# Optimization experiments

Measured on AMD Instinct MI355X. Metric: run time of the kernel, lower is better.

Reference implementation:

```python
import jax, jax.numpy as jnp
import numpy as np

N = 16384      # nodes (256 chess boards x 64 squares)
E = 393216     # edges (avg degree 24)
G = 256        # graphs
HID = 128
H = 4
C = 32         # head dim
L = 8          # 4 blocks x 2 GATv2Conv
NODE_DIM = 21
EDGE_DIM = 6


def setup_inputs() -> dict:
    key = jax.random.key(0)
    ks = jax.random.split(key, 12)
    x = jax.random.normal(ks[0], (N, NODE_DIM), jnp.float32)
    edge_index = jax.random.randint(ks[1], (2, E), 0, N, dtype=jnp.int32)
    edge_attr = jax.random.uniform(ks[2], (E, EDGE_DIM), dtype=jnp.float32)
    batch = jnp.sort(jax.random.randint(ks[3], (N,), 0, G, dtype=jnp.int32))

    def w(k, shape, fan_in):
        return jax.random.normal(k, shape, jnp.float32) * (1.0 / np.sqrt(fan_in))

    Win = w(ks[4], (NODE_DIM, HID), NODE_DIM)
    b_in = jnp.zeros((HID,), jnp.float32)
    Wl = w(ks[5], (L, HID, HID), HID)
    bl = jnp.zeros((L, HID), jnp.float32)
    Wr = w(ks[6], (L, HID, HID), HID)
    br = jnp.zeros((L, HID), jnp.float32)
    We = w(ks[7], (L, EDGE_DIM, HID), EDGE_DIM)
    att = w(ks[8], (L, H, C), C)
    bconv = jnp.zeros((L, HID), jnp.float32)
    gamma = jnp.ones((L, HID), jnp.float32)
    beta = jnp.zeros((L, HID), jnp.float32)
    W1 = w(ks[9], (HID, 64), HID)
    b1 = jnp.zeros((64,), jnp.float32)
    W2 = w(ks[10], (64, 3), 64)
    b2 = jnp.zeros((3,), jnp.float32)
    return dict(x=x, edge_index=edge_index, edge_attr=edge_attr, batch=batch,
                Win=Win, b_in=b_in, Wl=Wl, bl=bl, Wr=Wr, br=br, We=We, att=att,
                bconv=bconv, gamma=gamma, beta=beta, W1=W1, b1=b1, W2=W2, b2=b2)


def _gatv2(h, src, dst, ea, Wl, bl, Wr, br, We, att, bias):
    # PyG GATv2Conv: message j->i uses x_j from lin_l, x_i from lin_r
    xl = (h @ Wl + bl).reshape(N, H, C)
    xr = (h @ Wr + br).reshape(N, H, C)
    ee = (ea @ We).reshape(-1, H, C)
    m = jax.nn.leaky_relu(xl[src] + xr[dst] + ee, 0.2)   # [Ef, H, C]
    s = jnp.einsum('ehc,hc->eh', m, att)                 # [Ef, H]
    smax = jax.ops.segment_max(s, dst, num_segments=N)   # self-loops => no empty segs
    ex = jnp.exp(s - smax[dst])
    den = jax.ops.segment_sum(ex, dst, num_segments=N)
    alpha = ex / den[dst]                                # edge softmax per target node
    out = jax.ops.segment_sum(alpha[:, :, None] * xl[src], dst, num_segments=N)
    return out.reshape(N, HID) + bias


def _bn(x, g, b):
    mu = jnp.mean(x, axis=0)
    var = jnp.var(x, axis=0)
    return g * (x - mu) * jax.lax.rsqrt(var + 1e-5) + b


def reference(x, edge_index, edge_attr, batch, Win, b_in, Wl, bl, Wr, br, We, att,
              bconv, gamma, beta, W1, b1, W2, b2):
    src0, dst0 = edge_index[0], edge_index[1]
    # add self-loops with fill_value='mean' (per-target mean of incoming edge_attr)
    deg = jax.ops.segment_sum(jnp.ones((E,), jnp.float32), dst0, num_segments=N)
    loop_attr = jax.ops.segment_sum(edge_attr, dst0, num_segments=N) / jnp.maximum(deg, 1.0)[:, None]
    idx = jnp.arange(N, dtype=src0.dtype)
    src = jnp.concatenate([src0, idx])
    dst = jnp.concatenate([dst0, idx])
    ea = jnp.concatenate([edge_attr, loop_attr], axis=0)

    h = jax.nn.relu(x @ Win + b_in)
    for blk in range(4):
        res = h
        l = 2 * blk
        h = jax.nn.relu(_bn(_gatv2(h, src, dst, ea, Wl[l], bl[l], Wr[l], br[l], We[l], att[l], bconv[l]), gamma[l], beta[l]))
        l = 2 * blk + 1
        h = _bn(_gatv2(h, src, dst, ea, Wl[l], bl[l], Wr[l], br[l], We[l], att[l], bconv[l]), gamma[l], beta[l])
        h = jax.nn.relu(h + res)

    cnt = jnp.maximum(jax.ops.segment_sum(jnp.ones((N,), jnp.float32), batch, num_segments=G), 1.0)
    pooled = jax.ops.segment_sum(h, batch, num_segments=G) / cnt[:, None]
    logits = jax.nn.relu(pooled @ W1 + b1) @ W2 + b2
    return logits
```

## Files before the change

kernel.cpp:

```cpp
#include <hip/hip_runtime.h>
#include <math.h>

constexpr int N   = 16384;
constexpr int E   = 393216;
constexpr int EF  = E + N;
constexpr int G   = 256;
constexpr int HID = 128;

__device__ __forceinline__ float red16(float x) {
    union fi { float f; int i; };
    fi a, b;
    a.f = x;
    b.i = __builtin_amdgcn_mov_dpp(a.i, 0x121, 0xf, 0xf, false); a.f += b.f;
    b.i = __builtin_amdgcn_mov_dpp(a.i, 0x122, 0xf, 0xf, false); a.f += b.f;
    b.i = __builtin_amdgcn_mov_dpp(a.i, 0x124, 0xf, 0xf, false); a.f += b.f;
    b.i = __builtin_amdgcn_mov_dpp(a.i, 0x128, 0xf, 0xf, false); a.f += b.f;
    return a.f;
}

__global__ __launch_bounds__(256) void k_hist(const int* __restrict__ dst,
                                              int* __restrict__ cnt) {
    int e = blockIdx.x * 256 + threadIdx.x;
    if (e < E) atomicAdd(&cnt[dst[e]], 1);
}

__global__ __launch_bounds__(1024) void k_scan(const int* __restrict__ cnt,
                                               int* __restrict__ row_ptr) {
    __shared__ int lds[1024];
    int t = threadIdx.x;
    int local[16];
    int s = 0;
    int base = t * 16;
#pragma unroll
    for (int q = 0; q < 16; q++) { local[q] = cnt[base + q] + 1; s += local[q]; }
    lds[t] = s;
    __syncthreads();
    for (int off = 1; off < 1024; off <<= 1) {
        int v = (t >= off) ? lds[t - off] : 0;
        __syncthreads();
        lds[t] += v;
        __syncthreads();
    }
    int run = (t == 0) ? 0 : lds[t - 1];
    if (t == 0) row_ptr[0] = 0;
#pragma unroll
    for (int q = 0; q < 16; q++) { run += local[q]; row_ptr[base + q + 1] = run; }
}

__global__ __launch_bounds__(256) void k_scatter(const int* __restrict__ src,
                                                 const int* __restrict__ dst,
                                                 const int* __restrict__ row_ptr,
                                                 int* __restrict__ fill,
                                                 int* __restrict__ csr_src,
                                                 int* __restrict__ csr_eid) {
    int e = blockIdx.x * 256 + threadIdx.x;
    if (e >= E) return;
    int d = dst[e];
    int pos = row_ptr[d] + atomicAdd(&fill[d], 1);
    csr_src[pos] = src[e];
    csr_eid[pos] = e;
}

__global__ __launch_bounds__(256) void k_selfloop(const int* __restrict__ row_ptr,
                                                  int* __restrict__ csr_src,
                                                  int* __restrict__ csr_eid) {
    int i = blockIdx.x * 256 + threadIdx.x;
    if (i >= N) return;
    int pos = row_ptr[i + 1] - 1;
    csr_src[pos] = i;
    csr_eid[pos] = E + i;
}

__global__ __launch_bounds__(256) void k_loopattr(const int* __restrict__ row_ptr,
                                                  const int* __restrict__ csr_eid,
                                                  const float* __restrict__ edge_attr,
                                                  float* __restrict__ loop_attr) {
    int i = blockIdx.x * 256 + threadIdx.x;
    if (i >= N) return;
    int e0 = row_ptr[i], e1 = row_ptr[i + 1] - 1;
    float s[6] = {0, 0, 0, 0, 0, 0};
    for (int e = e0; e < e1; e++) {
        int eid = csr_eid[e];
#pragma unroll
        for (int d = 0; d < 6; d++) s[d] += edge_attr[eid * 6 + d];
    }
    float deg = (float)(e1 - e0);
    float inv = 1.0f / fmaxf(deg, 1.0f);
#pragma unroll
    for (int d = 0; d < 6; d++) loop_attr[i * 6 + d] = s[d] * inv;
}

__global__ __launch_bounds__(256) void k_build_ea(const int* __restrict__ csr_eid,
                                                  const float* __restrict__ edge_attr,
                                                  const float* __restrict__ loop_attr,
                                                  float* __restrict__ csr_ea) {
    int p = blockIdx.x * 256 + threadIdx.x;
    if (p >= EF) return;
    int eid = csr_eid[p];
    const float* s = (eid < E) ? (edge_attr + (size_t)eid * 6)
                               : (loop_attr + (size_t)(eid - E) * 6);
    float4 a = {s[0], s[1], s[2], s[3]};
    float4 b = {s[4], s[5], 0.0f, 0.0f};
    float4* dst = (float4*)(csr_ea + (size_t)p * 8);
    dst[0] = a;
    dst[1] = b;
}

__global__ __launch_bounds__(128) void k_ingemm(const float* __restrict__ x,
                                                const float* __restrict__ Win,
                                                const float* __restrict__ b_in,
                                                float* __restrict__ h) {
    __shared__ float xs[21];
    int i = blockIdx.x;
    int c = threadIdx.x;
    if (c < 21) xs[c] = x[i * 21 + c];
    __syncthreads();
    float acc = b_in[c];
#pragma unroll
    for (int d = 0; d < 21; d++) acc += xs[d] * Win[d * HID + c];
    h[i * HID + c] = fmaxf(acc, 0.0f);
}

__global__ __launch_bounds__(256) void k_gemm_lr(const float* __restrict__ h,
                                                 const float* __restrict__ Wl,
                                                 const float* __restrict__ bl,
                                                 const float* __restrict__ Wr,
                                                 const float* __restrict__ br,
                                                 float* __restrict__ XL,
                                                 float* __restrict__ XR) {
    __shared__ float hs[16][HID];
    int t = threadIdx.x;
    int r0 = blockIdx.x * 16;
    {
        int row = t >> 4;
        int col = (t & 15) * 8;
        const float4* src = (const float4*)&h[(size_t)(r0 + row) * HID + col];
        float4* dst = (float4*)&hs[row][col];
        dst[0] = src[0];
        dst[1] = src[1];
    }
    __syncthreads();
    bool right = t >= 128;
    int cp = (t & 63) * 2;
    int rbase = ((t >> 6) & 1) * 8;
    const float* W    = right ? Wr : Wl;
    const float* bias = right ? br : bl;
    float* OUT        = right ? XR : XL;
    float b0 = bias[cp], b1 = bias[cp + 1];
    float acc0[8], acc1[8];
#pragma unroll
    for (int r = 0; r < 8; r++) { acc0[r] = b0; acc1[r] = b1; }
    for (int k = 0; k < HID; k += 4) {
        float4 h4[8];
#pragma unroll
        for (int r = 0; r < 8; r++) h4[r] = *(const float4*)&hs[rbase + r][k];
#pragma unroll
        for (int kk = 0; kk < 4; kk++) {
            float2 w = *(const float2*)&W[(size_t)(k + kk) * HID + cp];
#pragma unroll
            for (int r = 0; r < 8; r++) {
                float hv = ((const float*)&h4[r])[kk];
                acc0[r] = fmaf(hv, w.x, acc0[r]);
                acc1[r] = fmaf(hv, w.y, acc1[r]);
            }
        }
    }
#pragma unroll
    for (int r = 0; r < 8; r++) {
        float2 o = {acc0[r], acc1[r]};
        *(float2*)&OUT[(size_t)(r0 + rbase + r) * HID + cp] = o;
    }
}

__global__ __launch_bounds__(256) void k_edge(const int* __restrict__ row_ptr,
                                              const int* __restrict__ csr_src,
                                              const float* __restrict__ csr_ea,
                                              const float* __restrict__ xl,
                                              const float* __restrict__ xr,
                                              const float* __restrict__ We_l,
                                              const float* __restrict__ att_l,
                                              float* __restrict__ gout) {
    int wave = (blockIdx.x * blockDim.x + threadIdx.x) >> 6;
    int lane = threadIdx.x & 63;
    if (wave >= N) return;
    int i = wave;
    int hh = lane >> 4;
    int ss = lane & 15;
    int ch0 = hh * 32 + 2 * ss;

    float2 xr2 = *(const float2*)&xr[(size_t)i * HID + ch0];
    float a0 = att_l[ch0], a1 = att_l[ch0 + 1];
    float we0[6], we1[6];
#pragma unroll
    for (int d = 0; d < 6; d++) {
        float2 w = *(const float2*)&We_l[d * HID + ch0];
        we0[d] = w.x;
        we1[d] = w.y;
    }

    float rm = -INFINITY, rd = 0.0f, acc0 = 0.0f, acc1 = 0.0f;

    int e0 = __builtin_amdgcn_readfirstlane(row_ptr[i]);
    int e1 = __builtin_amdgcn_readfirstlane(row_ptr[i + 1]);

    for (int e = e0; e < e1; e += 4) {
        float p[4], v0[4], v1[4];
#pragma unroll
        for (int k = 0; k < 4; k++) {
            int ee = e + k;
            int ec = (ee < e1) ? ee : (e1 - 1);
            int j = __builtin_amdgcn_readfirstlane(csr_src[ec]);
            const float4* ea4 = (const float4*)(csr_ea + (size_t)ec * 8);
            float4 eaA = ea4[0];
            float4 eaB = ea4[1];
            float2 xl2 = *(const float2*)&xl[(size_t)j * HID + ch0];
            float s0 = eaA.x * we0[0], s1 = eaA.x * we1[0];
            s0 = fmaf(eaA.y, we0[1], s0); s1 = fmaf(eaA.y, we1[1], s1);
            s0 = fmaf(eaA.z, we0[2], s0); s1 = fmaf(eaA.z, we1[2], s1);
            s0 = fmaf(eaA.w, we0[3], s0); s1 = fmaf(eaA.w, we1[3], s1);
            s0 = fmaf(eaB.x, we0[4], s0); s1 = fmaf(eaB.x, we1[4], s1);
            s0 = fmaf(eaB.y, we0[5], s0); s1 = fmaf(eaB.y, we1[5], s1);
            float m0 = xl2.x + xr2.x + s0;
            float m1 = xl2.y + xr2.y + s1;
            m0 = fmaxf(m0, 0.2f * m0);
            m1 = fmaxf(m1, 0.2f * m1);
            float pv = m0 * a0;
            pv = fmaf(m1, a1, pv);
            pv = red16(pv);
            p[k] = (ee < e1) ? pv : -INFINITY;
            v0[k] = xl2.x;
            v1[k] = xl2.y;
        }
        float bm = fmaxf(fmaxf(p[0], p[1]), fmaxf(p[2], p[3]));
        float nm = fmaxf(rm, bm);
        float sc = __expf(rm - nm);
        rd *= sc; acc0 *= sc; acc1 *= sc;
#pragma unroll
        for (int k = 0; k < 4; k++) {
            float ek = __expf(p[k] - nm);
            rd += ek;
            acc0 = fmaf(ek, v0[k], acc0);
            acc1 = fmaf(ek, v1[k], acc1);
        }
        rm = nm;
    }
    float inv = 1.0f / rd;
    float2 o = {acc0 * inv, acc1 * inv};
    *(float2*)&gout[(size_t)i * HID + ch0] = o;
}

__global__ __launch_bounds__(256) void k_bnstats(const float* __restrict__ v,
                                                 float* __restrict__ sums) {
    __shared__ float l_s[256], l_q[256];
    int t = threadIdx.x;
    int c = t & 127;
    int half = t >> 7;
    int r = blockIdx.x * 128 + half;
    float s = 0.0f, q = 0.0f;
    for (int it = 0; it < 64; it++, r += 2) {
        float val = v[(size_t)r * HID + c];
        s += val;
        q += val * val;
    }
    l_s[t] = s; l_q[t] = q;
    __syncthreads();
    if (t < 128) {
        s = l_s[t] + l_s[t + 128];
        q = l_q[t] + l_q[t + 128];
        atomicAdd(&sums[c], s);
        atomicAdd(&sums[128 + c], q);
    }
}

__global__ __launch_bounds__(256) void k_bnapply(const float* __restrict__ g,
                                                 const float* __restrict__ sums,
                                                 const float* __restrict__ gamma,
                                                 const float* __restrict__ beta,
                                                 const float* __restrict__ res,
                                                 float* __restrict__ out) {
    int idx4 = (blockIdx.x * 256 + threadIdx.x) * 4;
    int c = idx4 & 127;
    const float invN = 1.0f / (float)N;
    float4 gv = *(const float4*)&g[idx4];
    float4 s4 = *(const float4*)&sums[c];
    float4 q4 = *(const float4*)&sums[128 + c];
    float4 gm = *(const float4*)&gamma[c];
    float4 bt = *(const float4*)&beta[c];
    float4 o;
    {
        float mean = s4.x * invN, var = q4.x * invN - mean * mean;
        o.x = gm.x * (gv.x - mean) * rsqrtf(var + 1e-5f) + bt.x;
        mean = s4.y * invN; var = q4.y * invN - mean * mean;
        o.y = gm.y * (gv.y - mean) * rsqrtf(var + 1e-5f) + bt.y;
        mean = s4.z * invN; var = q4.z * invN - mean * mean;
        o.z = gm.z * (gv.z - mean) * rsqrtf(var + 1e-5f) + bt.z;
        mean = s4.w * invN; var = q4.w * invN - mean * mean;
        o.w = gm.w * (gv.w - mean) * rsqrtf(var + 1e-5f) + bt.w;
    }
    if (res) {
        float4 r4 = *(const float4*)&res[idx4];
        o.x += r4.x; o.y += r4.y; o.z += r4.z; o.w += r4.w;
    }
    o.x = fmaxf(o.x, 0.0f);
    o.y = fmaxf(o.y, 0.0f);
    o.z = fmaxf(o.z, 0.0f);
    o.w = fmaxf(o.w, 0.0f);
    *(float4*)&out[idx4] = o;
}

__global__ __launch_bounds__(128) void k_pool(const float* __restrict__ h,
                                              const int* __restrict__ batch,
                                              const float* __restrict__ W1,
                                              const float* __restrict__ b1,
                                              const float* __restrict__ W2,
                                              const float* __restrict__ b2,
                                              float* __restrict__ out) {
    __shared__ float pooled[HID];
    __shared__ float hid[64];
    __shared__ int bounds[2];
    int g = blockIdx.x;
    int t = threadIdx.x;
    if (t < 2) {
        int target = g + t;
        int lo = 0, hi = N;
        while (lo < hi) {
            int mid = (lo + hi) >> 1;
            if (batch[mid] < target) lo = mid + 1; else hi = mid;
        }
        bounds[t] = lo;
    }
    __syncthreads();
    int s = bounds[0], e = bounds[1];
    float acc = 0.0f;
    for (int r = s; r < e; r++) acc += h[(size_t)r * HID + t];
    float cntf = fmaxf((float)(e - s), 1.0f);
    pooled[t] = acc / cntf;
    __syncthreads();
    if (t < 64) {
        float a = b1[t];
#pragma unroll 4
        for (int c = 0; c < HID; c++) a += pooled[c] * W1[c * 64 + t];
        hid[t] = fmaxf(a, 0.0f);
    }
    __syncthreads();
    if (t < 3) {
        float a = b2[t];
#pragma unroll
        for (int j = 0; j < 64; j++) a += hid[j] * W2[j * 3 + t];
        out[g * 3 + t] = a;
    }
}

extern "C" void kernel_launch(void* const* d_in, const int* in_sizes, int n_in,
                              void* d_out, int out_size, void* d_ws, size_t ws_size,
                              hipStream_t stream) {
    const float* x         = (const float*)d_in[0];
    const int*   edge_index= (const int*)d_in[1];
    const float* edge_attr = (const float*)d_in[2];
    const int*   batch     = (const int*)d_in[3];
    const float* Win       = (const float*)d_in[4];
    const float* b_in      = (const float*)d_in[5];
    const float* Wl        = (const float*)d_in[6];
    const float* bl        = (const float*)d_in[7];
    const float* Wr        = (const float*)d_in[8];
    const float* br        = (const float*)d_in[9];
    const float* We        = (const float*)d_in[10];
    const float* att       = (const float*)d_in[11];
    const float* gamma     = (const float*)d_in[13];
    const float* beta      = (const float*)d_in[14];
    const float* W1        = (const float*)d_in[15];
    const float* b1        = (const float*)d_in[16];
    const float* W2        = (const float*)d_in[17];
    const float* b2        = (const float*)d_in[18];
    float* out = (float*)d_out;

    const int* src0 = edge_index;
    const int* dst0 = edge_index + E;

    char* ws = (char*)d_ws;
    size_t off = 0;
    auto alloc = [&](size_t bytes) -> void* {
        void* p = ws + off;
        off += (bytes + 255) & ~(size_t)255;
        return p;
    };
    int*   cnt       = (int*)alloc((size_t)2 * N * sizeof(int));
    int*   fill      = cnt + N;
    float* bnsums    = (float*)alloc((size_t)8 * 256 * sizeof(float));
    int*   row_ptr   = (int*)alloc((size_t)(N + 1) * sizeof(int));
    int*   csr_src   = (int*)alloc((size_t)EF * sizeof(int));
    int*   csr_eid   = (int*)alloc((size_t)EF * sizeof(int));
    float* csr_ea    = (float*)alloc((size_t)EF * 8 * sizeof(float));
    float* loop_attr = (float*)alloc((size_t)N * 6 * sizeof(float));
    float* H0        = (float*)alloc((size_t)N * HID * sizeof(float));
    float* H1        = (float*)alloc((size_t)N * HID * sizeof(float));
    float* XL        = (float*)alloc((size_t)N * HID * sizeof(float));
    float* XR        = (float*)alloc((size_t)N * HID * sizeof(float));
    float* GOUT      = (float*)alloc((size_t)N * HID * sizeof(float));

    hipMemsetAsync(cnt, 0, (size_t)2 * N * sizeof(int) + 8 * 256 * sizeof(float),
                   stream);
    k_hist<<<(E + 255) / 256, 256, 0, stream>>>(dst0, cnt);
    k_scan<<<1, 1024, 0, stream>>>(cnt, row_ptr);
    k_scatter<<<(E + 255) / 256, 256, 0, stream>>>(src0, dst0, row_ptr, fill,
                                                   csr_src, csr_eid);
    k_selfloop<<<(N + 255) / 256, 256, 0, stream>>>(row_ptr, csr_src, csr_eid);
    k_loopattr<<<(N + 255) / 256, 256, 0, stream>>>(row_ptr, csr_eid, edge_attr,
                                                    loop_attr);
    k_build_ea<<<(EF + 255) / 256, 256, 0, stream>>>(csr_eid, edge_attr,
                                                     loop_attr, csr_ea);
    k_ingemm<<<N, 128, 0, stream>>>(x, Win, b_in, H0);

    for (int l = 0; l < 8; l++) {
        const float* hin = (l % 2 == 0) ? H0 : H1;
        k_gemm_lr<<<N / 16, 256, 0, stream>>>(hin,
                                              Wl + (size_t)l * HID * HID, bl + l * HID,
                                              Wr + (size_t)l * HID * HID, br + l * HID,
                                              XL, XR);
        k_edge<<<N / 4, 256, 0, stream>>>(row_ptr, csr_src, csr_ea,
                                          XL, XR,
                                          We + (size_t)l * 6 * HID,
                                          att + (size_t)l * HID, GOUT);
        float* bns = bnsums + l * 256;
        k_bnstats<<<128, 256, 0, stream>>>(GOUT, bns);
        if (l % 2 == 0) {
            k_bnapply<<<(N * HID) / 1024, 256, 0, stream>>>(GOUT, bns,
                                                            gamma + l * HID,
                                                            beta + l * HID,
                                                            nullptr, H1);
        } else {
            k_bnapply<<<(N * HID) / 1024, 256, 0, stream>>>(GOUT, bns,
                                                            gamma + l * HID,
                                                            beta + l * HID,
                                                            H0, H0);
        }
    }
    k_pool<<<G, 128, 0, stream>>>(H0, batch, W1, b1, W2, b2, out);
}
```

Measured before the change: 753.8 us.

## Fuse BN-apply into GEMM, prefetch xl gathers, fold loop-attr into histogram

The even-layer BatchNorm+ReLU is now applied inside the next layer's k_gemm_lr while it loads the tile into LDS. This drops one full-tensor bnapply pass and the H1 buffer. The edge kernel double-buffers the xl gathers four edges ahead so the loads overlap with the softmax math. The self-loop attribute sum is computed with atomics in k_hist, removing the k_loopattr kernel, and k_bnstats uses 256 blocks instead of 128. The cost is extra float atomics and recomputing the BN scale and shift in every GEMM block.

```diff
diff --git a/kernel.cpp b/kernel.cpp
--- a/kernel.cpp
+++ b/kernel.cpp
@@ -19,9 +19,16 @@
 }
 
 __global__ __launch_bounds__(256) void k_hist(const int* __restrict__ dst,
-                                              int* __restrict__ cnt) {
+                                              const float* __restrict__ edge_attr,
+                                              int* __restrict__ cnt,
+                                              float* __restrict__ loopsum) {
     int e = blockIdx.x * 256 + threadIdx.x;
-    if (e < E) atomicAdd(&cnt[dst[e]], 1);
+    if (e >= E) return;
+    int d = dst[e];
+    atomicAdd(&cnt[d], 1);
+#pragma unroll
+    for (int q = 0; q < 6; q++)
+        atomicAdd(&loopsum[d * 6 + q], edge_attr[e * 6 + q]);
 }
 
 __global__ __launch_bounds__(1024) void k_scan(const int* __restrict__ cnt,
@@ -71,36 +78,27 @@
     csr_eid[pos] = E + i;
 }
 
-__global__ __launch_bounds__(256) void k_loopattr(const int* __restrict__ row_ptr,
-                                                  const int* __restrict__ csr_eid,
+__global__ __launch_bounds__(256) void k_build_ea(const int* __restrict__ csr_eid,
+                                                  const int* __restrict__ row_ptr,
                                                   const float* __restrict__ edge_attr,
-                                                  float* __restrict__ loop_attr) {
-    int i = blockIdx.x * 256 + threadIdx.x;
-    if (i >= N) return;
-    int e0 = row_ptr[i], e1 = row_ptr[i + 1] - 1;
-    float s[6] = {0, 0, 0, 0, 0, 0};
-    for (int e = e0; e < e1; e++) {
-        int eid = csr_eid[e];
-#pragma unroll
-        for (int d = 0; d < 6; d++) s[d] += edge_attr[eid * 6 + d];
-    }
-    float deg = (float)(e1 - e0);
-    float inv = 1.0f / fmaxf(deg, 1.0f);
-#pragma unroll
-    for (int d = 0; d < 6; d++) loop_attr[i * 6 + d] = s[d] * inv;
-}
-
-__global__ __launch_bounds__(256) void k_build_ea(const int* __restrict__ csr_eid,
-                                                  const float* __restrict__ edge_attr,
-                                                  const float* __restrict__ loop_attr,
+                                                  const float* __restrict__ loopsum,
                                                   float* __restrict__ csr_ea) {
     int p = blockIdx.x * 256 + threadIdx.x;
     if (p >= EF) return;
     int eid = csr_eid[p];
-    const float* s = (eid < E) ? (edge_attr + (size_t)eid * 6)
-                               : (loop_attr + (size_t)(eid - E) * 6);
-    float4 a = {s[0], s[1], s[2], s[3]};
-    float4 b = {s[4], s[5], 0.0f, 0.0f};
+    float4 a, b;
+    if (eid < E) {
+        const float* s = edge_attr + (size_t)eid * 6;
+        a = {s[0], s[1], s[2], s[3]};
+        b = {s[4], s[5], 0.0f, 0.0f};
+    } else {
+        int i = eid - E;
+        float deg = (float)(row_ptr[i + 1] - row_ptr[i] - 1);
+        float inv = 1.0f / fmaxf(deg, 1.0f);
+        const float* s = loopsum + (size_t)i * 6;
+        a = {s[0] * inv, s[1] * inv, s[2] * inv, s[3] * inv};
+        b = {s[4] * inv, s[5] * inv, 0.0f, 0.0f};
+    }
     float4* dst = (float4*)(csr_ea + (size_t)p * 8);
     dst[0] = a;
     dst[1] = b;
@@ -122,6 +120,9 @@
 }
 
 __global__ __launch_bounds__(256) void k_gemm_lr(const float* __restrict__ h,
+                                                 const float* __restrict__ bns,
+                                                 const float* __restrict__ gamma,
+                                                 const float* __restrict__ beta,
                                                  const float* __restrict__ Wl,
                                                  const float* __restrict__ bl,
                                                  const float* __restrict__ Wr,
@@ -129,15 +130,44 @@
                                                  float* __restrict__ XL,
                                                  float* __restrict__ XR) {
     __shared__ float hs[16][HID];
+    __shared__ float sc[HID], sh[HID];
     int t = threadIdx.x;
     int r0 = blockIdx.x * 16;
+    if (bns) {
+        if (t < 128) {
+            const float invN = 1.0f / (float)N;
+            float mean = bns[t] * invN;
+            float var  = bns[128 + t] * invN - mean * mean;
+            float inv  = rsqrtf(var + 1e-5f);
+            float s = gamma[t] * inv;
+            sc[t] = s;
+            sh[t] = beta[t] - mean * s;
+        }
+        __syncthreads();
+    }
     {
         int row = t >> 4;
         int col = (t & 15) * 8;
         const float4* src = (const float4*)&h[(size_t)(r0 + row) * HID + col];
+        float4 a = src[0];
+        float4 b = src[1];
+        if (bns) {
+            float4 s0 = *(const float4*)&sc[col];
+            float4 s1 = *(const float4*)&sc[col + 4];
+            float4 h0 = *(const float4*)&sh[col];
+            float4 h1 = *(const float4*)&sh[col + 4];
+            a.x = fmaxf(fmaf(a.x, s0.x, h0.x), 0.0f);
+            a.y = fmaxf(fmaf(a.y, s0.y, h0.y), 0.0f);
+            a.z = fmaxf(fmaf(a.z, s0.z, h0.z), 0.0f);
+            a.w = fmaxf(fmaf(a.w, s0.w, h0.w), 0.0f);
+            b.x = fmaxf(fmaf(b.x, s1.x, h1.x), 0.0f);
+            b.y = fmaxf(fmaf(b.y, s1.y, h1.y), 0.0f);
+            b.z = fmaxf(fmaf(b.z, s1.z, h1.z), 0.0f);
+            b.w = fmaxf(fmaf(b.w, s1.w, h1.w), 0.0f);
+        }
         float4* dst = (float4*)&hs[row][col];
-        dst[0] = src[0];
-        dst[1] = src[1];
+        dst[0] = a;
+        dst[1] = b;
     }
     __syncthreads();
     bool right = t >= 128;
@@ -169,6 +199,18 @@
     for (int r = 0; r < 8; r++) {
         float2 o = {acc0[r], acc1[r]};
         *(float2*)&OUT[(size_t)(r0 + rbase + r) * HID + cp] = o;
+    }
+}
+
+__device__ __forceinline__ void pf_xl(int e, int e1,
+                                      const int* __restrict__ csr_src,
+                                      const float* __restrict__ xl, int ch0,
+                                      float2 out[4]) {
+#pragma unroll
+    for (int k = 0; k < 4; k++) {
+        int ec = (e + k < e1) ? e + k : e1 - 1;
+        int j = __builtin_amdgcn_readfirstlane(csr_src[ec]);
+        out[k] = *(const float2*)&xl[(size_t)j * HID + ch0];
     }
 }
 
@@ -203,33 +245,29 @@
     int e0 = __builtin_amdgcn_readfirstlane(row_ptr[i]);
     int e1 = __builtin_amdgcn_readfirstlane(row_ptr[i + 1]);
 
-    for (int e = e0; e < e1; e += 4) {
-        float p[4], v0[4], v1[4];
+    auto body = [&](int e, const float2 xlv[4]) {
+        float p[4];
 #pragma unroll
         for (int k = 0; k < 4; k++) {
             int ee = e + k;
             int ec = (ee < e1) ? ee : (e1 - 1);
-            int j = __builtin_amdgcn_readfirstlane(csr_src[ec]);
             const float4* ea4 = (const float4*)(csr_ea + (size_t)ec * 8);
             float4 eaA = ea4[0];
             float4 eaB = ea4[1];
-            float2 xl2 = *(const float2*)&xl[(size_t)j * HID + ch0];
             float s0 = eaA.x * we0[0], s1 = eaA.x * we1[0];
             s0 = fmaf(eaA.y, we0[1], s0); s1 = fmaf(eaA.y, we1[1], s1);
             s0 = fmaf(eaA.z, we0[2], s0); s1 = fmaf(eaA.z, we1[2], s1);
             s0 = fmaf(eaA.w, we0[3], s0); s1 = fmaf(eaA.w, we1[3], s1);
             s0 = fmaf(eaB.x, we0[4], s0); s1 = fmaf(eaB.x, we1[4], s1);
             s0 = fmaf(eaB.y, we0[5], s0); s1 = fmaf(eaB.y, we1[5], s1);
-            float m0 = xl2.x + xr2.x + s0;
-            float m1 = xl2.y + xr2.y + s1;
+            float m0 = xlv[k].x + xr2.x + s0;
+            float m1 = xlv[k].y + xr2.y + s1;
             m0 = fmaxf(m0, 0.2f * m0);
             m1 = fmaxf(m1, 0.2f * m1);
             float pv = m0 * a0;
             pv = fmaf(m1, a1, pv);
             pv = red16(pv);
             p[k] = (ee < e1) ? pv : -INFINITY;
-            v0[k] = xl2.x;
-            v1[k] = xl2.y;
         }
         float bm = fmaxf(fmaxf(p[0], p[1]), fmaxf(p[2], p[3]));
         float nm = fmaxf(rm, bm);
@@ -239,10 +277,19 @@
         for (int k = 0; k < 4; k++) {
             float ek = __expf(p[k] - nm);
             rd += ek;
-            acc0 = fmaf(ek, v0[k], acc0);
-            acc1 = fmaf(ek, v1[k], acc1);
+            acc0 = fmaf(ek, xlv[k].x, acc0);
+            acc1 = fmaf(ek, xlv[k].y, acc1);
         }
         rm = nm;
+    };
+
+    float2 bufA[4], bufB[4];
+    pf_xl(e0, e1, csr_src, xl, ch0, bufA);
+    for (int e = e0; e < e1; e += 8) {
+        pf_xl(e + 4, e1, csr_src, xl, ch0, bufB);
+        body(e, bufA);
+        pf_xl(e + 8, e1, csr_src, xl, ch0, bufA);
+        if (e + 4 < e1) body(e + 4, bufB);
     }
     float inv = 1.0f / rd;
     float2 o = {acc0 * inv, acc1 * inv};
@@ -255,9 +302,9 @@
     int t = threadIdx.x;
     int c = t & 127;
     int half = t >> 7;
-    int r = blockIdx.x * 128 + half;
+    int r = blockIdx.x * 64 + half;
     float s = 0.0f, q = 0.0f;
-    for (int it = 0; it < 64; it++, r += 2) {
+    for (int it = 0; it < 32; it++, r += 2) {
         float val = v[(size_t)r * HID + c];
         s += val;
         q += val * val;
@@ -297,14 +344,11 @@
         mean = s4.w * invN; var = q4.w * invN - mean * mean;
         o.w = gm.w * (gv.w - mean) * rsqrtf(var + 1e-5f) + bt.w;
     }
-    if (res) {
-        float4 r4 = *(const float4*)&res[idx4];
-        o.x += r4.x; o.y += r4.y; o.z += r4.z; o.w += r4.w;
-    }
-    o.x = fmaxf(o.x, 0.0f);
-    o.y = fmaxf(o.y, 0.0f);
-    o.z = fmaxf(o.z, 0.0f);
-    o.w = fmaxf(o.w, 0.0f);
+    float4 r4 = *(const float4*)&res[idx4];
+    o.x = fmaxf(o.x + r4.x, 0.0f);
+    o.y = fmaxf(o.y + r4.y, 0.0f);
+    o.z = fmaxf(o.z + r4.z, 0.0f);
+    o.w = fmaxf(o.w + r4.w, 0.0f);
     *(float4*)&out[idx4] = o;
 }
 
@@ -387,33 +431,35 @@
     int*   cnt       = (int*)alloc((size_t)2 * N * sizeof(int));
     int*   fill      = cnt + N;
     float* bnsums    = (float*)alloc((size_t)8 * 256 * sizeof(float));
+    float* loopsum   = (float*)alloc((size_t)N * 6 * sizeof(float));
     int*   row_ptr   = (int*)alloc((size_t)(N + 1) * sizeof(int));
     int*   csr_src   = (int*)alloc((size_t)EF * sizeof(int));
     int*   csr_eid   = (int*)alloc((size_t)EF * sizeof(int));
     float* csr_ea    = (float*)alloc((size_t)EF * 8 * sizeof(float));
-    float* loop_attr = (float*)alloc((size_t)N * 6 * sizeof(float));
     float* H0        = (float*)alloc((size_t)N * HID * sizeof(float));
-    float* H1        = (float*)alloc((size_t)N * HID * sizeof(float));
     float* XL        = (float*)alloc((size_t)N * HID * sizeof(float));
     float* XR        = (float*)alloc((size_t)N * HID * sizeof(float));
     float* GOUT      = (float*)alloc((size_t)N * HID * sizeof(float));
 
-    hipMemsetAsync(cnt, 0, (size_t)2 * N * sizeof(int) + 8 * 256 * sizeof(float),
-                   stream);
-    k_hist<<<(E + 255) / 256, 256, 0, stream>>>(dst0, cnt);
+    size_t zbytes = (size_t)2 * N * sizeof(int) + 8 * 256 * sizeof(float)
+                  + (size_t)N * 6 * sizeof(float);
+    hipMemsetAsync(cnt, 0, zbytes, stream);
+    k_hist<<<(E + 255) / 256, 256, 0, stream>>>(dst0, edge_attr, cnt, loopsum);
     k_scan<<<1, 1024, 0, stream>>>(cnt, row_ptr);
     k_scatter<<<(E + 255) / 256, 256, 0, stream>>>(src0, dst0, row_ptr, fill,
                                                    csr_src, csr_eid);
     k_selfloop<<<(N + 255) / 256, 256, 0, stream>>>(row_ptr, csr_src, csr_eid);
-    k_loopattr<<<(N + 255) / 256, 256, 0, stream>>>(row_ptr, csr_eid, edge_attr,
-                                                    loop_attr);
-    k_build_ea<<<(EF + 255) / 256, 256, 0, stream>>>(csr_eid, edge_attr,
-                                                     loop_attr, csr_ea);
+    k_build_ea<<<(EF + 255) / 256, 256, 0, stream>>>(csr_eid, row_ptr, edge_attr,
+                                                     loopsum, csr_ea);
     k_ingemm<<<N, 128, 0, stream>>>(x, Win, b_in, H0);
 
     for (int l = 0; l < 8; l++) {
-        const float* hin = (l % 2 == 0) ? H0 : H1;
-        k_gemm_lr<<<N / 16, 256, 0, stream>>>(hin,
+        bool odd = (l & 1) != 0;
+        const float* hin = odd ? GOUT : H0;
+        const float* bns_in = odd ? (bnsums + (l - 1) * 256) : nullptr;
+        const float* g_in  = odd ? (gamma + (l - 1) * HID) : nullptr;
+        const float* b_in2 = odd ? (beta  + (l - 1) * HID) : nullptr;
+        k_gemm_lr<<<N / 16, 256, 0, stream>>>(hin, bns_in, g_in, b_in2,
                                               Wl + (size_t)l * HID * HID, bl + l * HID,
                                               Wr + (size_t)l * HID * HID, br + l * HID,
                                               XL, XR);
@@ -422,13 +468,8 @@
                                           We + (size_t)l * 6 * HID,
                                           att + (size_t)l * HID, GOUT);
         float* bns = bnsums + l * 256;
-        k_bnstats<<<128, 256, 0, stream>>>(GOUT, bns);
-        if (l % 2 == 0) {
-            k_bnapply<<<(N * HID) / 1024, 256, 0, stream>>>(GOUT, bns,
-                                                            gamma + l * HID,
-                                                            beta + l * HID,
-                                                            nullptr, H1);
-        } else {
+        k_bnstats<<<256, 256, 0, stream>>>(GOUT, bns);
+        if (odd) {
             k_bnapply<<<(N * HID) / 1024, 256, 0, stream>>>(GOUT, bns,
                                                             gamma + l * HID,
                                                             beta + l * HID,
```

After: 869.5 us. 1.15x slower.
